# Optimization experiments

Measured on AMD Instinct MI355X. Metric: run time of the kernel, lower is better.

## Reference

```python
import jax, jax.numpy as jnp
import numpy as np

N_NODES = 50000
N_EDGES = 800000
NUM_GRAPHS = 64
F_IN, F_HID, F_HID2, F_OUT = 128, 96, 48, 32


def gcn_conv(x, W, b, src, dst, n_nodes):
    # PyG GCNConv: h = x @ W; out = D^{-1/2} (A+I) D^{-1/2} h + b
    # src/dst already include self loops; degree computed on dst.
    h = x @ W  # [N, F_out]
    deg = jax.ops.segment_sum(jnp.ones(dst.shape[0], dtype=h.dtype), dst, num_segments=n_nodes)
    dinv = jax.lax.rsqrt(deg)  # deg >= 1 due to self loops
    norm = dinv[src] * dinv[dst]  # [E]
    msg = h[src] * norm[:, None]  # gather + scale
    out = jax.ops.segment_sum(msg, dst, num_segments=n_nodes)  # scatter-add
    return out + b


def setup_inputs() -> dict:
    key = jax.random.key(0)
    ks = jax.random.split(key, 10)
    x = jax.random.normal(ks[0], (N_NODES, F_IN), dtype=jnp.float32)
    edge_index = jax.random.randint(ks[1], (2, N_EDGES), 0, N_NODES, dtype=jnp.int64)
    batch = jnp.sort(jax.random.randint(ks[2], (N_NODES,), 0, NUM_GRAPHS, dtype=jnp.int64))
    def glorot(k, fi, fo):
        s = np.sqrt(6.0 / (fi + fo)).astype(np.float32)
        return jax.random.uniform(k, (fi, fo), dtype=jnp.float32, minval=-s, maxval=s)
    W1 = glorot(ks[3], F_IN, F_HID)
    b1 = jnp.zeros((F_HID,), dtype=jnp.float32)
    W2 = glorot(ks[4], F_HID, F_HID2)
    b2 = jnp.zeros((F_HID2,), dtype=jnp.float32)
    W3 = glorot(ks[5], F_HID2, F_OUT)
    b3 = jnp.zeros((F_OUT,), dtype=jnp.float32)
    return {"x": x, "edge_index": edge_index, "batch": batch,
            "W1": W1, "b1": b1, "W2": W2, "b2": b2, "W3": W3, "b3": b3}


def reference(x, edge_index, batch, W1, b1, W2, b2, W3, b3):
    n = x.shape[0]
    loops = jnp.arange(n, dtype=edge_index.dtype)
    src = jnp.concatenate([edge_index[0], loops])
    dst = jnp.concatenate([edge_index[1], loops])

    h = jax.nn.relu(gcn_conv(x, W1, b1, src, dst, n))
    h = jax.nn.relu(gcn_conv(h, W2, b2, src, dst, n))
    h = jax.nn.relu(gcn_conv(h, W3, b3, src, dst, n))

    # global mean pool over graphs in the batch
    sums = jax.ops.segment_sum(h, batch, num_segments=NUM_GRAPHS)
    cnt = jax.ops.segment_sum(jnp.ones((n,), dtype=h.dtype), batch, num_segments=NUM_GRAPHS)
    return sums / jnp.maximum(cnt, 1.0)[:, None]
```

## Files before the change

kernel.cpp:

```cpp
#include <hip/hip_runtime.h>

#define N_NODES 50000
#define N_EDGES 800000
#define NUM_GRAPHS 64

#define CAPLOG 6
#define CAP    (1 << CAPLOG)
#define ZROW   N_NODES

__device__ __forceinline__ float bf_lo(unsigned u) { return __uint_as_float(u << 16); }
__device__ __forceinline__ float bf_hi(unsigned u) { return __uint_as_float(u & 0xffff0000u); }
__device__ __forceinline__ unsigned short f2bf(float f) {
    unsigned u = __float_as_uint(f);
    return (unsigned short)((u + 0x7fffu + ((u >> 16) & 1u)) >> 16);
}

template<int S>
__device__ __forceinline__ void agg_row8(const unsigned short* __restrict__ Hc,
                                         const unsigned short* __restrict__ csr,
                                         int node, int m, float a[8]) {
    uint4 sv = *(const uint4*)(Hc + (size_t)node * S);
    a[0] = bf_lo(sv.x); a[1] = bf_hi(sv.x); a[2] = bf_lo(sv.y); a[3] = bf_hi(sv.y);
    a[4] = bf_lo(sv.z); a[5] = bf_hi(sv.z); a[6] = bf_lo(sv.w); a[7] = bf_hi(sv.w);
    const int e0 = node << CAPLOG, e1 = e0 + m;
    for (int e = e0; e < e1; e += 4) {
        ushort4 ss = *(const ushort4*)&csr[e];
        int s0 = ss.x;
        int s1 = (e + 1 < e1) ? (int)ss.y : ZROW;
        int s2 = (e + 2 < e1) ? (int)ss.z : ZROW;
        int s3 = (e + 3 < e1) ? (int)ss.w : ZROW;
        uint4 v0 = *(const uint4*)(Hc + (size_t)s0 * S);
        uint4 v1 = *(const uint4*)(Hc + (size_t)s1 * S);
        uint4 v2 = *(const uint4*)(Hc + (size_t)s2 * S);
        uint4 v3 = *(const uint4*)(Hc + (size_t)s3 * S);
        a[0] += bf_lo(v0.x) + bf_lo(v1.x) + bf_lo(v2.x) + bf_lo(v3.x);
        a[1] += bf_hi(v0.x) + bf_hi(v1.x) + bf_hi(v2.x) + bf_hi(v3.x);
        a[2] += bf_lo(v0.y) + bf_lo(v1.y) + bf_lo(v2.y) + bf_lo(v3.y);
        a[3] += bf_hi(v0.y) + bf_hi(v1.y) + bf_hi(v2.y) + bf_hi(v3.y);
        a[4] += bf_lo(v0.z) + bf_lo(v1.z) + bf_lo(v2.z) + bf_lo(v3.z);
        a[5] += bf_hi(v0.z) + bf_hi(v1.z) + bf_hi(v2.z) + bf_hi(v3.z);
        a[6] += bf_lo(v0.w) + bf_lo(v1.w) + bf_lo(v2.w) + bf_lo(v3.w);
        a[7] += bf_hi(v0.w) + bf_hi(v1.w) + bf_hi(v2.w) + bf_hi(v3.w);
    }
}

#define SC_NG    4
#define SC_BPG   256
#define SC_GRID  (SC_NG * SC_BPG)
#define NPG      ((N_NODES + SC_NG - 1) / SC_NG)
#define GEMM_NBX ((N_NODES + 63) / 64)
#define GEMM_NB  (GEMM_NBX * 2)
#define FUSE_GRID (SC_GRID + 1 + GEMM_NB)

__global__ __launch_bounds__(192) void k_scatgemm(
        const int* __restrict__ ei, int* __restrict__ cnt,
        unsigned short* __restrict__ csr,
        const int* __restrict__ batch, int* __restrict__ start,
        const float* __restrict__ X, const float* __restrict__ W,
        float* __restrict__ Hraw) {
    const int bid = blockIdx.x;
    const int tid = threadIdx.x;

    int role, idx;
    if (bid < 2 * SC_GRID) { role = bid & 1; idx = bid >> 1; }
    else if (bid == 2 * SC_GRID) {
        if (tid <= NUM_GRAPHS) {
            int lo = 0, hi = N_NODES;
            while (lo < hi) {
                int mid = (lo + hi) >> 1;
                if (batch[mid] < tid) lo = mid + 1; else hi = mid;
            }
            start[tid] = lo;
        }
        return;
    }
    else { role = 1; idx = SC_GRID + (bid - 2 * SC_GRID - 1); }

    if (role == 0) {
        const int g  = idx & (SC_NG - 1);
        const int b  = idx / SC_NG;
        const int lo = g * NPG, hi = lo + NPG;
        const int* __restrict__ dst = ei + N_EDGES;
        for (int e = b * 192 + tid; e < N_EDGES; e += 192 * SC_BPG) {
            int d = dst[e];
            if (d >= lo && d < hi) {
                int old = atomicAdd(&cnt[d], 1);
                if (old < CAP) csr[(d << CAPLOG) + old] = (unsigned short)ei[e];
            }
        }
        return;
    }

    const int bx = idx % GEMM_NBX;
    const int by = idx / GEMM_NBX;
    const int n0 = bx * 64;
    const int c0 = by * 48;
    __shared__ float ws[64 * 48];

    const int ft = tid % 12;
    const int nt = tid / 12;
    const float* xp[4];
    #pragma unroll
    for (int i = 0; i < 4; ++i) {
        int node = n0 + nt * 4 + i;
        int nc = node < N_NODES ? node : N_NODES - 1;
        xp[i] = X + (size_t)nc * 128;
    }
    float acc[4][4];
    #pragma unroll
    for (int i = 0; i < 4; ++i) { acc[i][0] = acc[i][1] = acc[i][2] = acc[i][3] = 0.f; }

    for (int kh = 0; kh < 2; ++kh) {
        __syncthreads();
        for (int i = tid; i < 64 * 48 / 4; i += 192) {
            int k = i / 12, cv = i % 12;
            *(float4*)&ws[k * 48 + cv * 4] =
                *(const float4*)&W[(kh * 64 + k) * 96 + c0 + cv * 4];
        }
        __syncthreads();
        const int kb = kh * 64;
        for (int k = 0; k < 64; k += 4) {
            float4 w0 = *(const float4*)&ws[(k + 0) * 48 + ft * 4];
            float4 w1 = *(const float4*)&ws[(k + 1) * 48 + ft * 4];
            float4 w2 = *(const float4*)&ws[(k + 2) * 48 + ft * 4];
            float4 w3 = *(const float4*)&ws[(k + 3) * 48 + ft * 4];
            #pragma unroll
            for (int i = 0; i < 4; ++i) {
                float4 xv = *(const float4*)(xp[i] + kb + k);
                acc[i][0] += xv.x * w0.x + xv.y * w1.x + xv.z * w2.x + xv.w * w3.x;
                acc[i][1] += xv.x * w0.y + xv.y * w1.y + xv.z * w2.y + xv.w * w3.y;
                acc[i][2] += xv.x * w0.z + xv.y * w1.z + xv.z * w2.z + xv.w * w3.z;
                acc[i][3] += xv.x * w0.w + xv.y * w1.w + xv.z * w2.w + xv.w * w3.w;
            }
        }
    }
    #pragma unroll
    for (int i = 0; i < 4; ++i) {
        int node = n0 + nt * 4 + i;
        if (node < N_NODES)
            *(float4*)&Hraw[(size_t)node * 96 + c0 + ft * 4] =
                make_float4(acc[i][0], acc[i][1], acc[i][2], acc[i][3]);
    }
}

__global__ __launch_bounds__(256) void k_scale(
        const float* __restrict__ Hraw, const int* __restrict__ cnt,
        unsigned short* __restrict__ H1) {
    const int NQ = (N_NODES + 1) * 24;
    for (int q = blockIdx.x * 256 + threadIdx.x; q < NQ; q += gridDim.x * 256) {
        int n = q / 24, c = (q % 24) * 4;
        if (n == ZROW) {
            *(ushort4*)&H1[(size_t)n * 96 + c] = make_ushort4(0, 0, 0, 0);
            continue;
        }
        float s = rsqrtf((float)(cnt[n] + 1));
        float4 v = *(const float4*)&Hraw[(size_t)n * 96 + c];
        ushort4 o;
        o.x = f2bf(v.x * s); o.y = f2bf(v.y * s);
        o.z = f2bf(v.z * s); o.w = f2bf(v.w * s);
        *(ushort4*)&H1[(size_t)n * 96 + c] = o;
    }
}

__global__ __launch_bounds__(384) void k_agg12(
        const unsigned short* __restrict__ H1, const int* __restrict__ cnt,
        const unsigned short* __restrict__ csr, const float* __restrict__ b1,
        const float* __restrict__ W2, unsigned short* __restrict__ H2) {
    __shared__ float Ws[96 * 48];
    __shared__ float T[32][97];
    __shared__ float dinvS[32];
    const int t = threadIdx.x;
    for (int i = t; i < 1152; i += 384)
        *(float4*)&Ws[i * 4] = *(const float4*)&W2[i * 4];

    if (blockIdx.x == 0 && t < 16) {
        ushort4 z = make_ushort4(0, 0, 0, 0);
        *(ushort4*)&H2[(size_t)ZROW * 64 + t * 4] = z;
    }

    const int n_l = t / 12, c = t % 12;
    const int node = blockIdx.x * 32 + n_l;
    if (node < N_NODES) {
        int deg = cnt[node];
        float d = rsqrtf((float)(deg + 1));
        if (c == 0) dinvS[n_l] = d;
        float a[8];
        agg_row8<96>(H1 + c * 8, csr, node, min(deg, CAP), a);
        const float4* bp = (const float4*)(b1 + c * 8);
        float4 b0 = bp[0], bb1 = bp[1];
        float* Tr = &T[n_l][c * 8];
        Tr[0] = fmaxf(a[0] * d + b0.x, 0.f);  Tr[1] = fmaxf(a[1] * d + b0.y, 0.f);
        Tr[2] = fmaxf(a[2] * d + b0.z, 0.f);  Tr[3] = fmaxf(a[3] * d + b0.w, 0.f);
        Tr[4] = fmaxf(a[4] * d + bb1.x, 0.f); Tr[5] = fmaxf(a[5] * d + bb1.y, 0.f);
        Tr[6] = fmaxf(a[6] * d + bb1.z, 0.f); Tr[7] = fmaxf(a[7] * d + bb1.w, 0.f);
    }
    __syncthreads();

    const int n2 = t / 12;
    const int f0 = (t % 12) * 4;
    const int gn = blockIdx.x * 32 + n2;
    if (gn < N_NODES) {
        float4 acc = make_float4(0.f, 0.f, 0.f, 0.f);
        for (int k = 0; k < 96; ++k) {
            float tv = T[n2][k];
            float4 wv = *(const float4*)&Ws[k * 48 + f0];
            acc.x += tv * wv.x; acc.y += tv * wv.y; acc.z += tv * wv.z; acc.w += tv * wv.w;
        }
        float s2 = dinvS[n2];
        ushort4 o;
        o.x = f2bf(acc.x * s2); o.y = f2bf(acc.y * s2);
        o.z = f2bf(acc.z * s2); o.w = f2bf(acc.w * s2);
        *(ushort4*)&H2[(size_t)gn * 64 + f0] = o;
    }
}

__global__ __launch_bounds__(384) void k_agg23(
        const unsigned short* __restrict__ H2, const int* __restrict__ cnt,
        const unsigned short* __restrict__ csr, const float* __restrict__ b2,
        const float* __restrict__ W3, unsigned short* __restrict__ H3) {
    __shared__ float Ws[48 * 32];
    __shared__ float T[64][49];
    __shared__ float dinvS[64];
    const int t = threadIdx.x;
    for (int i = t; i < 384; i += 384)
        *(float4*)&Ws[i * 4] = *(const float4*)&W3[i * 4];

    if (blockIdx.x == 0 && t < 8) {
        ushort4 z = make_ushort4(0, 0, 0, 0);
        *(ushort4*)&H3[(size_t)ZROW * 32 + t * 4] = z;
    }

    const int n_l = t / 6, c = t % 6;
    const int node = blockIdx.x * 64 + n_l;
    if (node < N_NODES) {
        int deg = cnt[node];
        float d = rsqrtf((float)(deg + 1));
        if (c == 0) dinvS[n_l] = d;
        float a[8];
        agg_row8<64>(H2 + c * 8, csr, node, min(deg, CAP), a);
        const float4* bp = (const float4*)(b2 + c * 8);
        float4 b0 = bp[0], bb1 = bp[1];
        float* Tr = &T[n_l][c * 8];
        Tr[0] = fmaxf(a[0] * d + b0.x, 0.f);  Tr[1] = fmaxf(a[1] * d + b0.y, 0.f);
        Tr[2] = fmaxf(a[2] * d + b0.z, 0.f);  Tr[3] = fmaxf(a[3] * d + b0.w, 0.f);
        Tr[4] = fmaxf(a[4] * d + bb1.x, 0.f); Tr[5] = fmaxf(a[5] * d + bb1.y, 0.f);
        Tr[6] = fmaxf(a[6] * d + bb1.z, 0.f); Tr[7] = fmaxf(a[7] * d + bb1.w, 0.f);
    }
    __syncthreads();

    for (int vid = t; vid < 512; vid += 384) {
        const int n2 = vid / 8;
        const int f0 = (vid % 8) * 4;
        const int gn = blockIdx.x * 64 + n2;
        if (gn < N_NODES) {
            float4 acc = make_float4(0.f, 0.f, 0.f, 0.f);
            for (int k = 0; k < 48; ++k) {
                float tv = T[n2][k];
                float4 wv = *(const float4*)&Ws[k * 32 + f0];
                acc.x += tv * wv.x; acc.y += tv * wv.y; acc.z += tv * wv.z; acc.w += tv * wv.w;
            }
            float s3 = dinvS[n2];
            ushort4 o;
            o.x = f2bf(acc.x * s3); o.y = f2bf(acc.y * s3);
            o.z = f2bf(acc.z * s3); o.w = f2bf(acc.w * s3);
            *(ushort4*)&H3[(size_t)gn * 32 + f0] = o;
        }
    }
}

__global__ __launch_bounds__(256) void k_agg3p(
        const unsigned short* __restrict__ H3, const int* __restrict__ cnt,
        const unsigned short* __restrict__ csr, const float* __restrict__ b3,
        const int* __restrict__ batch, const int* __restrict__ start,
        float* __restrict__ gsum) {
    __shared__ float T[64][33];
    __shared__ float R[8][32];
    const int t = threadIdx.x;
    const int base = blockIdx.x * 64;

    const int n_l = t / 4, c = t % 4;
    const int node = base + n_l;
    if (node < N_NODES) {
        int deg = cnt[node];
        float d = rsqrtf((float)(deg + 1));
        float a[8];
        agg_row8<32>(H3 + c * 8, csr, node, min(deg, CAP), a);
        const float4* bp = (const float4*)(b3 + c * 8);
        float4 b0 = bp[0], b1 = bp[1];
        float* Tr = &T[n_l][c * 8];
        Tr[0] = fmaxf(a[0] * d + b0.x, 0.f); Tr[1] = fmaxf(a[1] * d + b0.y, 0.f);
        Tr[2] = fmaxf(a[2] * d + b0.z, 0.f); Tr[3] = fmaxf(a[3] * d + b0.w, 0.f);
        Tr[4] = fmaxf(a[4] * d + b1.x, 0.f); Tr[5] = fmaxf(a[5] * d + b1.y, 0.f);
        Tr[6] = fmaxf(a[6] * d + b1.z, 0.f); Tr[7] = fmaxf(a[7] * d + b1.w, 0.f);
    }
    __syncthreads();

    const int g_lo = batch[base < N_NODES ? base : N_NODES - 1];
    const int last = base + 63 < N_NODES ? base + 63 : N_NODES - 1;
    const int g_hi = batch[last];
    const int f = t & 31, k = t >> 5;
    for (int g = g_lo; g <= g_hi; ++g) {
        int r_lo = start[g] - base;     if (r_lo < 0) r_lo = 0;
        int r_hi = start[g + 1] - base; if (r_hi > 64) r_hi = 64;
        float p = 0.f;
        for (int r = r_lo + k; r < r_hi; r += 8) p += T[r][f];
        R[k][f] = p;
        __syncthreads();
        if (k == 0) {
            float s = R[0][f] + R[1][f] + R[2][f] + R[3][f]
                    + R[4][f] + R[5][f] + R[6][f] + R[7][f];
            if (r_hi > r_lo) atomicAdd(&gsum[g * 32 + f], s);
        }
        __syncthreads();
    }
}

__global__ void k_final(const float* __restrict__ gsum, const int* __restrict__ start,
                        float* __restrict__ out) {
    int t = blockIdx.x * blockDim.x + threadIdx.x;
    if (t < NUM_GRAPHS * 32) {
        int g = t >> 5;
        float c = (float)(start[g + 1] - start[g]);
        out[t] = gsum[t] / fmaxf(c, 1.0f);
    }
}

extern "C" void kernel_launch(void* const* d_in, const int* in_sizes, int n_in,
                              void* d_out, int out_size, void* d_ws, size_t ws_size,
                              hipStream_t stream) {
    const float* x     = (const float*)d_in[0];
    const int*   ei    = (const int*)d_in[1];
    const int*   batch = (const int*)d_in[2];
    const float* W1    = (const float*)d_in[3];
    const float* b1    = (const float*)d_in[4];
    const float* W2    = (const float*)d_in[5];
    const float* b2    = (const float*)d_in[6];
    const float* W3    = (const float*)d_in[7];
    const float* b3    = (const float*)d_in[8];
    float* out = (float*)d_out;

    char* ws = (char*)d_ws;
    size_t o = 0;
    auto alloc = [&](size_t bytes) {
        char* p = ws + o;
        o = (o + bytes + 255) & ~(size_t)255;
        return p;
    };
    unsigned short* H1 = (unsigned short*)alloc((size_t)(N_NODES + 1) * 96 * 2);
    unsigned short* H2 = (unsigned short*)alloc((size_t)(N_NODES + 1) * 64 * 2);
    unsigned short* H3 = (unsigned short*)alloc((size_t)(N_NODES + 1) * 32 * 2);
    float* H1raw  = (float*)alloc((size_t)N_NODES * 96 * 4);
    int*   cnt    = (int*)alloc((size_t)N_NODES * 4);
    unsigned short* csr = (unsigned short*)alloc((size_t)N_NODES * CAP * 2);
    int*   start  = (int*)alloc((NUM_GRAPHS + 1) * 4);
    float* gsum   = (float*)alloc((size_t)NUM_GRAPHS * 32 * 4);

    hipMemsetAsync(cnt, 0, (size_t)N_NODES * 4, stream);
    hipMemsetAsync(gsum, 0, (size_t)NUM_GRAPHS * 32 * 4, stream);

    hipLaunchKernelGGL(k_scatgemm, dim3(FUSE_GRID), dim3(192), 0, stream,
                       ei, cnt, csr, batch, start, x, W1, H1raw);
    hipLaunchKernelGGL(k_scale, dim3(2048), dim3(256), 0, stream, H1raw, cnt, H1);
    hipLaunchKernelGGL(k_agg12, dim3((N_NODES + 31) / 32), dim3(384), 0, stream,
                       H1, cnt, csr, b1, W2, H2);
    hipLaunchKernelGGL(k_agg23, dim3((N_NODES + 63) / 64), dim3(384), 0, stream,
                       H2, cnt, csr, b2, W3, H3);
    hipLaunchKernelGGL(k_agg3p, dim3((N_NODES + 63) / 64), dim3(256), 0, stream,
                       H3, cnt, csr, b3, batch, start, gsum);
    hipLaunchKernelGGL(k_final, dim3((NUM_GRAPHS * 32 + 255) / 256), dim3(256), 0, stream,
                       gsum, start, out);
}
```

Baseline: 210.5 us.

## Make scatter+GEMM kernel persistent with atomic ticket work queue for GEMM tiles

Replaces the role-split grid, where separate blocks did scatter, batch-start search or GEMM, with a fixed grid of 1024 blocks of 256 threads. Each block first does its share of the CSR edge scatter, then pulls GEMM tiles and the batch-start task from a global atomic ticket counter until the work runs out. The aim is fewer block launches and better load balance across the scatter and GEMM phases. In exchange it adds a ticket memset launch, a per-tile atomic plus barriers, and leaves 64 of 256 threads idle during GEMM tiles.

```diff
diff --git a/kernel.cpp b/kernel.cpp
--- a/kernel.cpp
+++ b/kernel.cpp
@@ -50,96 +50,101 @@
 #define NPG      ((N_NODES + SC_NG - 1) / SC_NG)
 #define GEMM_NBX ((N_NODES + 63) / 64)
 #define GEMM_NB  (GEMM_NBX * 2)
-#define FUSE_GRID (SC_GRID + 1 + GEMM_NB)
-
-__global__ __launch_bounds__(192) void k_scatgemm(
+#define N_TICKETS (1 + GEMM_NB)
+
+__global__ __launch_bounds__(256) void k_fused(
         const int* __restrict__ ei, int* __restrict__ cnt,
         unsigned short* __restrict__ csr,
         const int* __restrict__ batch, int* __restrict__ start,
         const float* __restrict__ X, const float* __restrict__ W,
-        float* __restrict__ Hraw) {
-    const int bid = blockIdx.x;
+        float* __restrict__ Hraw, int* __restrict__ ticket) {
+    __shared__ float ws[64 * 48];
+    __shared__ int tkt;
     const int tid = threadIdx.x;
 
-    int role, idx;
-    if (bid < 2 * SC_GRID) { role = bid & 1; idx = bid >> 1; }
-    else if (bid == 2 * SC_GRID) {
-        if (tid <= NUM_GRAPHS) {
-            int lo = 0, hi = N_NODES;
-            while (lo < hi) {
-                int mid = (lo + hi) >> 1;
-                if (batch[mid] < tid) lo = mid + 1; else hi = mid;
-            }
-            start[tid] = lo;
-        }
-        return;
-    }
-    else { role = 1; idx = SC_GRID + (bid - 2 * SC_GRID - 1); }
-
-    if (role == 0) {
-        const int g  = idx & (SC_NG - 1);
-        const int b  = idx / SC_NG;
+    {
+        const int g  = blockIdx.x & (SC_NG - 1);
+        const int b  = blockIdx.x / SC_NG;
         const int lo = g * NPG, hi = lo + NPG;
         const int* __restrict__ dst = ei + N_EDGES;
-        for (int e = b * 192 + tid; e < N_EDGES; e += 192 * SC_BPG) {
+        for (int e = b * 256 + tid; e < N_EDGES; e += 256 * SC_BPG) {
             int d = dst[e];
             if (d >= lo && d < hi) {
                 int old = atomicAdd(&cnt[d], 1);
                 if (old < CAP) csr[(d << CAPLOG) + old] = (unsigned short)ei[e];
             }
         }
-        return;
-    }
-
-    const int bx = idx % GEMM_NBX;
-    const int by = idx / GEMM_NBX;
-    const int n0 = bx * 64;
-    const int c0 = by * 48;
-    __shared__ float ws[64 * 48];
-
-    const int ft = tid % 12;
-    const int nt = tid / 12;
-    const float* xp[4];
-    #pragma unroll
-    for (int i = 0; i < 4; ++i) {
-        int node = n0 + nt * 4 + i;
-        int nc = node < N_NODES ? node : N_NODES - 1;
-        xp[i] = X + (size_t)nc * 128;
-    }
-    float acc[4][4];
-    #pragma unroll
-    for (int i = 0; i < 4; ++i) { acc[i][0] = acc[i][1] = acc[i][2] = acc[i][3] = 0.f; }
-
-    for (int kh = 0; kh < 2; ++kh) {
+    }
+
+    while (true) {
+        if (tid == 0) tkt = atomicAdd(ticket, 1);
         __syncthreads();
-        for (int i = tid; i < 64 * 48 / 4; i += 192) {
-            int k = i / 12, cv = i % 12;
-            *(float4*)&ws[k * 48 + cv * 4] =
-                *(const float4*)&W[(kh * 64 + k) * 96 + c0 + cv * 4];
-        }
-        __syncthreads();
-        const int kb = kh * 64;
-        for (int k = 0; k < 64; k += 4) {
-            float4 w0 = *(const float4*)&ws[(k + 0) * 48 + ft * 4];
-            float4 w1 = *(const float4*)&ws[(k + 1) * 48 + ft * 4];
-            float4 w2 = *(const float4*)&ws[(k + 2) * 48 + ft * 4];
-            float4 w3 = *(const float4*)&ws[(k + 3) * 48 + ft * 4];
+        const int t = tkt;
+        if (t >= N_TICKETS) break;
+
+        if (t == 0) {
+            if (tid <= NUM_GRAPHS) {
+                int lo = 0, hi = N_NODES;
+                while (lo < hi) {
+                    int mid = (lo + hi) >> 1;
+                    if (batch[mid] < tid) lo = mid + 1; else hi = mid;
+                }
+                start[tid] = lo;
+            }
+        } else {
+            const int gidx = t - 1;
+            const int bx = gidx % GEMM_NBX;
+            const int by = gidx / GEMM_NBX;
+            const int n0 = bx * 64;
+            const int c0 = by * 48;
+            const int ft = tid % 12;
+            const int nt = tid / 12;
+            const float* xp[4];
+            float acc[4][4];
             #pragma unroll
             for (int i = 0; i < 4; ++i) {
-                float4 xv = *(const float4*)(xp[i] + kb + k);
-                acc[i][0] += xv.x * w0.x + xv.y * w1.x + xv.z * w2.x + xv.w * w3.x;
-                acc[i][1] += xv.x * w0.y + xv.y * w1.y + xv.z * w2.y + xv.w * w3.y;
-                acc[i][2] += xv.x * w0.z + xv.y * w1.z + xv.z * w2.z + xv.w * w3.z;
-                acc[i][3] += xv.x * w0.w + xv.y * w1.w + xv.z * w2.w + xv.w * w3.w;
-            }
-        }
-    }
-    #pragma unroll
-    for (int i = 0; i < 4; ++i) {
-        int node = n0 + nt * 4 + i;
-        if (node < N_NODES)
-            *(float4*)&Hraw[(size_t)node * 96 + c0 + ft * 4] =
-                make_float4(acc[i][0], acc[i][1], acc[i][2], acc[i][3]);
+                acc[i][0] = acc[i][1] = acc[i][2] = acc[i][3] = 0.f;
+                int node = n0 + nt * 4 + i;
+                int nc = node < N_NODES ? node : N_NODES - 1;
+                xp[i] = X + (size_t)nc * 128;
+            }
+            for (int kh = 0; kh < 2; ++kh) {
+                __syncthreads();
+                for (int i = tid; i < 64 * 48 / 4; i += 256) {
+                    int k = i / 12, cv = i % 12;
+                    *(float4*)&ws[k * 48 + cv * 4] =
+                        *(const float4*)&W[(kh * 64 + k) * 96 + c0 + cv * 4];
+                }
+                __syncthreads();
+                if (nt < 16) {
+                    const int kb = kh * 64;
+                    for (int k = 0; k < 64; k += 4) {
+                        float4 w0 = *(const float4*)&ws[(k + 0) * 48 + ft * 4];
+                        float4 w1 = *(const float4*)&ws[(k + 1) * 48 + ft * 4];
+                        float4 w2 = *(const float4*)&ws[(k + 2) * 48 + ft * 4];
+                        float4 w3 = *(const float4*)&ws[(k + 3) * 48 + ft * 4];
+                        #pragma unroll
+                        for (int i = 0; i < 4; ++i) {
+                            float4 xv = *(const float4*)(xp[i] + kb + k);
+                            acc[i][0] += xv.x * w0.x + xv.y * w1.x + xv.z * w2.x + xv.w * w3.x;
+                            acc[i][1] += xv.x * w0.y + xv.y * w1.y + xv.z * w2.y + xv.w * w3.y;
+                            acc[i][2] += xv.x * w0.z + xv.y * w1.z + xv.z * w2.z + xv.w * w3.z;
+                            acc[i][3] += xv.x * w0.w + xv.y * w1.w + xv.z * w2.w + xv.w * w3.w;
+                        }
+                    }
+                }
+            }
+            if (nt < 16) {
+                #pragma unroll
+                for (int i = 0; i < 4; ++i) {
+                    int node = n0 + nt * 4 + i;
+                    if (node < N_NODES)
+                        *(float4*)&Hraw[(size_t)node * 96 + c0 + ft * 4] =
+                            make_float4(acc[i][0], acc[i][1], acc[i][2], acc[i][3]);
+                }
+            }
+        }
+        __syncthreads();
     }
 }
 
@@ -354,12 +359,14 @@
     unsigned short* csr = (unsigned short*)alloc((size_t)N_NODES * CAP * 2);
     int*   start  = (int*)alloc((NUM_GRAPHS + 1) * 4);
     float* gsum   = (float*)alloc((size_t)NUM_GRAPHS * 32 * 4);
+    int*   ticket = (int*)alloc(4);
 
     hipMemsetAsync(cnt, 0, (size_t)N_NODES * 4, stream);
     hipMemsetAsync(gsum, 0, (size_t)NUM_GRAPHS * 32 * 4, stream);
-
-    hipLaunchKernelGGL(k_scatgemm, dim3(FUSE_GRID), dim3(192), 0, stream,
-                       ei, cnt, csr, batch, start, x, W1, H1raw);
+    hipMemsetAsync(ticket, 0, 4, stream);
+
+    hipLaunchKernelGGL(k_fused, dim3(SC_GRID), dim3(256), 0, stream,
+                       ei, cnt, csr, batch, start, x, W1, H1raw, ticket);
     hipLaunchKernelGGL(k_scale, dim3(2048), dim3(256), 0, stream, H1raw, cnt, H1);
     hipLaunchKernelGGL(k_agg12, dim3((N_NODES + 31) / 32), dim3(384), 0, stream,
                        H1, cnt, csr, b1, W2, H2);
```

Result: slower. 227.5 us (+8.1%).
